# Optimization experiments

Measured on AMD Instinct MI355X. Metric: run time of the kernel, lower is better.

## Reference

```python
import jax, jax.numpy as jnp
import numpy as np
from jax import lax

RATE, STRIDE, KSIZE, FUSE_K, SCALE = 2, 1, 3, 3, 10.0


def img2col(img, k, s):
    # torch F.unfold with padding=1, reshaped to [B, L, C, k, k] (L row-major over patch grid)
    B, C, H, W = img.shape
    p = jnp.pad(img, ((0, 0), (0, 0), (1, 1), (1, 1)))
    nH = (H + 2 - k) // s + 1
    nW = (W + 2 - k) // s + 1
    slabs = [p[:, :, ki:ki + s * (nH - 1) + 1:s, kj:kj + s * (nW - 1) + 1:s]
             for ki in range(k) for kj in range(k)]
    pats = jnp.stack(slabs, axis=2).reshape(B, C, k, k, nH, nW)
    return pats.transpose(0, 4, 5, 1, 2, 3).reshape(B, nH * nW, C, k, k)


def diag_prop(M, fk):
    # conv2d of the [L, L] score matrix with an identity fuse kernel == sum over diagonal shifts
    r = fk // 2
    B, L, _ = M.shape
    Mp = jnp.pad(M, ((0, 0), (r, r), (r, r)))
    out = jnp.zeros_like(M)
    for d in range(-r, r + 1):
        out = out + Mp[:, r + d:r + d + L, r + d:r + d + L]
    return out


def _fwd(foreground, background, mask):
    pad = KSIZE // 2
    # raw-resolution background patches used for reconstruction: [B, L, C, 2*rate, 2*rate]
    cols = img2col(background, 2 * RATE, RATE * STRIDE)
    # nearest-neighbor downsample by rate (torch F.interpolate scale_factor=1/rate, mode='nearest')
    fg = foreground[:, :, ::RATE, ::RATE]
    bg = background[:, :, ::RATE, ::RATE]
    m = mask[:, :, ::RATE, ::RATE]
    mask_cols = img2col(m, KSIZE, STRIDE)            # [B, L, 1, 3, 3]
    masked = jnp.sum(mask_cols, axis=(2, 3, 4)) == 0.0  # [B, L]
    kern = img2col(bg, KSIZE, STRIDE)                # [B, L, C, 3, 3]
    denom = jnp.sqrt(jnp.sum(kern * kern, axis=(2, 3, 4), keepdims=True))
    kern = kern / jnp.maximum(denom, 1e-3)

    def conv_one(img, k_):  # img [C,h,w], k_ [L,C,3,3] -> [L,h,w]
        return lax.conv_general_dilated(img[None], k_, (1, 1), [(pad, pad), (pad, pad)],
                                        dimension_numbers=('NCHW', 'OIHW', 'NCHW'))[0]

    scores = jax.vmap(conv_one)(fg, kern)            # [B, L, h, w]
    B, L, h, w = scores.shape
    # attention propagation: identity-kernel conv over [h*w, h*w], both orientations
    M = diag_prop(scores.reshape(B, L, h * w), FUSE_K)
    M = M.reshape(B, h, w, h, w).transpose(0, 2, 1, 4, 3).reshape(B, h * w, h * w)
    M = diag_prop(M, FUSE_K)
    scores = M.reshape(B, h, w, h, w).transpose(0, 2, 1, 4, 3).reshape(B, L, h, w)
    scores = jnp.where(masked[:, :, None, None], -1000.0, scores)
    soft = jax.nn.softmax(SCALE * scores, axis=1)

    kt = 2 * RATE
    tpad = kt - 1 - pad  # conv_transpose2d(stride=rate, padding=pad) as dilated conv

    def deconv_one(s_, t_):  # s_ [L,h,w], t_ [L,C,kt,kt] -> [C,H,W]
        W2 = jnp.flip(jnp.transpose(t_, (1, 0, 2, 3)), (2, 3))  # [C,L,kt,kt]
        return lax.conv_general_dilated(s_[None], W2, (1, 1), [(tpad, tpad), (tpad, tpad)],
                                        lhs_dilation=(RATE, RATE),
                                        dimension_numbers=('NCHW', 'OIHW', 'NCHW'))[0]

    return jax.vmap(deconv_one)(soft, cols)          # [B, C, H, W]


def setup_inputs() -> dict:
    key = jax.random.key(0)
    kf, kb, km = jax.random.split(key, 3)
    B, C, H, W = 2, 64, 128, 128
    foreground = jax.random.normal(kf, (B, C, H, W), jnp.float32)
    background = jax.random.normal(kb, (B, C, H, W), jnp.float32)
    mask = (jax.random.uniform(km, (B, 1, H, W)) > 0.5).astype(jnp.float32)
    return {"foreground": foreground, "background": background, "mask": mask}


def reference(foreground, background, mask):
    return _fwd(foreground, background, mask)
```

## Files before the change

### kernel.cpp

```cpp
#include <hip/hip_runtime.h>
#include <hip/hip_bf16.h>

#define B_ 2
#define C_ 64
#define H_ 128
#define W_ 128
#define HS 64
#define WS 64
#define L_ 4096
#define S_ 4096
#define K1_ 576
#define NCOL 1024
#define SCALE_ 10.0f

typedef __attribute__((ext_vector_type(8))) short bf16x8;
typedef __attribute__((ext_vector_type(8))) _Float16 f16x8;
typedef __attribute__((ext_vector_type(4))) float f32x4;

__device__ __forceinline__ void async_copy16(const void* gsrc, void* ldst) {
    __builtin_amdgcn_global_load_lds(
        (__attribute__((address_space(1))) const void*)gsrc,
        (__attribute__((address_space(3))) void*)ldst, 16, 0, 0);
}

__device__ __forceinline__ int TT(int x) { return ((x & 63) << 6) | (x >> 6); }

__device__ __forceinline__ float diag3Y(const float* __restrict__ Y, int l, int s) {
    int tl = TT(l), ts = TT(s);
    float acc = 0.f;
#pragma unroll
    for (int d2 = -1; d2 <= 1; ++d2) {
        int p = tl + d2, q = ts + d2;
        if ((unsigned)p < 4096u && (unsigned)q < 4096u)
            acc += Y[((size_t)TT(p) << 12) + TT(q)];
    }
    return acc;
}

__global__ void k_sumsq(const float* __restrict__ bg, float* __restrict__ ssq) {
    int idx = blockIdx.x * 256 + threadIdx.x;
    if (idx >= B_ * HS * WS) return;
    int pix = idx & 4095, b = idx >> 12;
    int i = pix >> 6, j = pix & 63;
    float ss = 0.f;
    for (int c = 0; c < C_; ++c) {
        float v = bg[((b * C_ + c) * H_ + 2 * i) * W_ + 2 * j];
        ss += v * v;
    }
    ssq[idx] = ss;
}

__global__ void k_patch_stats(const float* __restrict__ mask, const float* __restrict__ ssq,
                              float* __restrict__ denom_inv, float* __restrict__ maskedf) {
    int idx = blockIdx.x * 256 + threadIdx.x;
    if (idx >= B_ * L_) return;
    int b = idx >> 12, l = idx & 4095, lh = l >> 6, lw = l & 63;
    float msum = 0.f, ss = 0.f;
    for (int di = -1; di <= 1; ++di)
        for (int dj = -1; dj <= 1; ++dj) {
            int i = lh + di, j = lw + dj;
            if (i >= 0 && i < HS && j >= 0 && j < WS) {
                msum += mask[(b * H_ + 2 * i) * W_ + 2 * j];
                ss += ssq[(b << 12) + (i << 6) + j];
            }
        }
    maskedf[idx] = (msum == 0.0f) ? 1.0f : 0.0f;
    denom_inv[idx] = 1.0f / fmaxf(sqrtf(ss), 0.001f);
}

__global__ void k_prep(const float* __restrict__ bgb, const float* __restrict__ fgb,
                       _Float16* __restrict__ bcol, _Float16* __restrict__ fcol,
                       __hip_bfloat16* __restrict__ colsT) {
    int idx = blockIdx.x * 256 + threadIdx.x;
    if (idx < 2 * L_ * K1_) {
        int which = idx >= L_ * K1_;
        int id = which ? idx - L_ * K1_ : idx;
        const float* src = which ? fgb : bgb;
        _Float16* dst = which ? fcol : bcol;
        int k = id % K1_;
        int l = id / K1_;
        int c = k / 9, r = k - 9 * c;
        int r3 = r / 3;
        int di = r3 - 1, dj = r - 3 * r3 - 1;
        int i = (l >> 6) + di, j = (l & 63) + dj;
        float v = 0.f;
        if (i >= 0 && i < HS && j >= 0 && j < WS) v = src[(c * H_ + 2 * i) * W_ + 2 * j];
        dst[id] = (_Float16)v;
    } else {
        int id = idx - 2 * L_ * K1_;
        int l = id & 4095, n = id >> 12;
        int kj = n & 3, ki = (n >> 2) & 3, c = n >> 4;
        int y = 2 * (l >> 6) + ki - 1, x = 2 * (l & 63) + kj - 1;
        float v = 0.f;
        if (y >= 0 && y < H_ && x >= 0 && x < W_) v = bgb[(c * H_ + y) * W_ + x];
        colsT[id] = __float2bfloat16(v);
    }
}

__global__ __launch_bounds__(256) void k_gemm1_mfma(const _Float16* __restrict__ A,
                                                    const _Float16* __restrict__ Bm,
                                                    const float* __restrict__ dinv,
                                                    float* __restrict__ scores,
                                                    float* __restrict__ Y) {
    __shared__ __align__(16) char shraw[65 * 129 * 4];
    _Float16* As = (_Float16*)shraw;
    _Float16* Bs = As + 8192;
    int t = threadIdx.x, lane = t & 63, w = t >> 6;
    int wm = w & 1, wn = w >> 1;
    int M0 = blockIdx.y * 128, N0 = blockIdx.x * 128;
    f32x4 acc[4][4] = {};
    for (int k0 = 0; k0 < K1_; k0 += 64) {
#pragma unroll
        for (int rp = 0; rp < 4; ++rp) {
            int chunk = rp * 256 + t;
            int row = chunk >> 3;
            int kc = (chunk & 7) ^ (row & 7);
            async_copy16(A + (size_t)(M0 + row) * K1_ + k0 + kc * 8, &As[chunk * 8]);
        }
#pragma unroll
        for (int rp = 0; rp < 4; ++rp) {
            int chunk = rp * 256 + t;
            int row = chunk >> 3;
            int kc = (chunk & 7) ^ (row & 7);
            async_copy16(Bm + (size_t)(N0 + row) * K1_ + k0 + kc * 8, &Bs[chunk * 8]);
        }
        __syncthreads();
        int qc = lane >> 4, mr = lane & 15;
#pragma unroll
        for (int kk = 0; kk < 2; ++kk) {
            int c = kk * 4 + qc;
            f16x8 af[4], bfr[4];
#pragma unroll
            for (int i = 0; i < 4; ++i) {
                int ra = wm * 64 + i * 16 + mr;
                int rb = wn * 64 + i * 16 + mr;
                af[i] = *(const f16x8*)&As[ra * 64 + (c ^ (ra & 7)) * 8];
                bfr[i] = *(const f16x8*)&Bs[rb * 64 + (c ^ (rb & 7)) * 8];
            }
#pragma unroll
            for (int mt = 0; mt < 4; ++mt)
#pragma unroll
                for (int nt = 0; nt < 4; ++nt)
                    acc[mt][nt] = __builtin_amdgcn_mfma_f32_16x16x32_f16(af[mt], bfr[nt], acc[mt][nt], 0, 0, 0);
        }
        __syncthreads();
    }
    int col = lane & 15, rq = (lane >> 4) * 4;
#pragma unroll
    for (int mt = 0; mt < 4; ++mt)
#pragma unroll
        for (int r = 0; r < 4; ++r) {
            int ml = wm * 64 + mt * 16 + rq + r;
            bool rstrip = (ml <= 1) || (ml >= 126);
            float dv = dinv[M0 + ml];
#pragma unroll
            for (int nt = 0; nt < 4; ++nt) {
                int nl = wn * 64 + nt * 16 + col;
                bool cstrip = (nl <= 1) || (nl >= 126);
                if (rstrip || cstrip)
                    scores[((size_t)(M0 + ml) << 12) + N0 + nl] = acc[mt][nt][r] * dv;
            }
        }
    float* sm = (float*)shraw;
#pragma unroll
    for (int pass = 0; pass < 2; ++pass) {
        int lo = pass * 63;
        __syncthreads();
#pragma unroll
        for (int mt = 0; mt < 4; ++mt)
#pragma unroll
            for (int r = 0; r < 4; ++r) {
                int ml = wm * 64 + mt * 16 + rq + r;
                if (ml >= lo && ml <= lo + 64) {
                    float dv = dinv[M0 + ml];
#pragma unroll
                    for (int nt = 0; nt < 4; ++nt) {
                        int nl = wn * 64 + nt * 16 + col;
                        sm[(ml - lo) * 129 + nl] = acc[mt][nt][r] * dv;
                    }
                }
            }
        __syncthreads();
        int r0 = pass == 0 ? 1 : 64;
        for (int e = t; e < 63 * 128; e += 256) {
            int rr = r0 + (e >> 7);
            int cc = e & 127;
            if (cc < 1 || cc > 126) continue;
            int li = rr - lo;
            float y = sm[(li - 1) * 129 + cc - 1] + sm[li * 129 + cc] + sm[(li + 1) * 129 + cc + 1];
            Y[((size_t)(M0 + rr) << 12) + N0 + cc] = y;
        }
    }
}

__global__ void k_pass1_edge(const float* __restrict__ scores, float* __restrict__ Y) {
    int idx = blockIdx.x * 256 + threadIdx.x;
    int a, c;
    if (idx < 262144) {
        int ri = idx >> 12;
        a = (ri >> 1) * 128 + ((ri & 1) ? 127 : 0);
        c = idx & 4095;
    } else {
        int j = idx - 262144;
        int ci = j >> 12;
        c = (ci >> 1) * 128 + ((ci & 1) ? 127 : 0);
        a = j & 4095;
    }
    float acc = 0.f;
#pragma unroll
    for (int d = -1; d <= 1; ++d) {
        int aa = a + d, cc = c + d;
        if ((unsigned)aa < 4096u && (unsigned)cc < 4096u)
            acc += scores[((size_t)aa << 12) + cc];
    }
    Y[((size_t)a << 12) + c] = acc;
}

__global__ __launch_bounds__(256) void k_soft3(const float* __restrict__ Y,
                                               const float* __restrict__ maskedf,
                                               __hip_bfloat16* __restrict__ softT,
                                               float* __restrict__ pml, float* __restrict__ pz) {
    __shared__ float tile[64][65];
    __shared__ float red[16][64];
    __shared__ float mloc[64];
    int t = threadIdx.x;
    int sx4 = t & 15, lg = t >> 4;
    int bid = blockIdx.x;
    int swz = (bid & 7) * 512 + (bid >> 3);
    int dg = swz >> 6, pos = swz & 63;
    int by = pos, bx = (pos + dg) & 63;
    int s0 = bx * 64, l0 = by * 64;
    bool interior = (bx >= 1) && (bx <= 62) && (by >= 1) && (by <= 62);
    float p0 = -3.0e38f, p1 = -3.0e38f, p2 = -3.0e38f, p3 = -3.0e38f;
    if (interior) {
        float4 v[12];
        float mk[4];
#pragma unroll
        for (int j = 0; j < 4; ++j) {
            int lloc = lg + 16 * j;
#pragma unroll
            for (int d2 = 0; d2 < 3; ++d2) {
                const float* p = Y + ((size_t)(64 * (by + d2 - 1) + lloc) << 12) + 64 * (bx + d2 - 1) + 4 * sx4;
                v[j * 3 + d2] = *(const float4*)p;
            }
        }
#pragma unroll
        for (int j = 0; j < 4; ++j) mk[j] = maskedf[l0 + lg + 16 * j];
#pragma unroll
        for (int j = 0; j < 4; ++j) {
            int lloc = lg + 16 * j;
            float a0 = v[j * 3].x + v[j * 3 + 1].x + v[j * 3 + 2].x;
            float a1 = v[j * 3].y + v[j * 3 + 1].y + v[j * 3 + 2].y;
            float a2 = v[j * 3].z + v[j * 3 + 1].z + v[j * 3 + 2].z;
            float a3 = v[j * 3].w + v[j * 3 + 1].w + v[j * 3 + 2].w;
            if (mk[j] != 0.f) { a0 = -1000.f; a1 = -1000.f; a2 = -1000.f; a3 = -1000.f; }
            tile[lloc][4 * sx4 + 0] = a0;
            tile[lloc][4 * sx4 + 1] = a1;
            tile[lloc][4 * sx4 + 2] = a2;
            tile[lloc][4 * sx4 + 3] = a3;
            p0 = fmaxf(p0, a0); p1 = fmaxf(p1, a1); p2 = fmaxf(p2, a2); p3 = fmaxf(p3, a3);
        }
    } else {
#pragma unroll
        for (int j = 0; j < 4; ++j) {
            int lloc = lg + 16 * j;
            int l = l0 + lloc;
            bool mk = (maskedf[l] != 0.f);
            float a0 = mk ? -1000.f : diag3Y(Y, l, s0 + 4 * sx4 + 0);
            float a1 = mk ? -1000.f : diag3Y(Y, l, s0 + 4 * sx4 + 1);
            float a2 = mk ? -1000.f : diag3Y(Y, l, s0 + 4 * sx4 + 2);
            float a3 = mk ? -1000.f : diag3Y(Y, l, s0 + 4 * sx4 + 3);
            tile[lloc][4 * sx4 + 0] = a0;
            tile[lloc][4 * sx4 + 1] = a1;
            tile[lloc][4 * sx4 + 2] = a2;
            tile[lloc][4 * sx4 + 3] = a3;
            p0 = fmaxf(p0, a0); p1 = fmaxf(p1, a1); p2 = fmaxf(p2, a2); p3 = fmaxf(p3, a3);
        }
    }
    red[lg][4 * sx4 + 0] = p0;
    red[lg][4 * sx4 + 1] = p1;
    red[lg][4 * sx4 + 2] = p2;
    red[lg][4 * sx4 + 3] = p3;
    __syncthreads();
    if (t < 64) {
        float m = -3.0e38f;
#pragma unroll
        for (int g = 0; g < 16; ++g) m = fmaxf(m, red[g][t]);
        mloc[t] = m;
        pml[(size_t)(s0 + t) * 64 + by] = m;
    }
    __syncthreads();
    float m0 = mloc[4 * sx4 + 0], m1 = mloc[4 * sx4 + 1], m2 = mloc[4 * sx4 + 2], m3 = mloc[4 * sx4 + 3];
    float z0 = 0.f, z1 = 0.f, z2 = 0.f, z3 = 0.f;
#pragma unroll
    for (int j = 0; j < 4; ++j) {
        int lloc = lg + 16 * j;
        float e0 = __expf(SCALE_ * (tile[lloc][4 * sx4 + 0] - m0));
        float e1 = __expf(SCALE_ * (tile[lloc][4 * sx4 + 1] - m1));
        float e2 = __expf(SCALE_ * (tile[lloc][4 * sx4 + 2] - m2));
        float e3 = __expf(SCALE_ * (tile[lloc][4 * sx4 + 3] - m3));
        tile[lloc][4 * sx4 + 0] = e0;
        tile[lloc][4 * sx4 + 1] = e1;
        tile[lloc][4 * sx4 + 2] = e2;
        tile[lloc][4 * sx4 + 3] = e3;
        z0 += e0; z1 += e1; z2 += e2; z3 += e3;
    }
    red[lg][4 * sx4 + 0] = z0;
    red[lg][4 * sx4 + 1] = z1;
    red[lg][4 * sx4 + 2] = z2;
    red[lg][4 * sx4 + 3] = z3;
    __syncthreads();
    if (t < 64) {
        float zz = 0.f;
#pragma unroll
        for (int g = 0; g < 16; ++g) zz += red[g][t];
        pz[(size_t)(s0 + t) * 64 + by] = zz;
    }
#pragma unroll
    for (int pp = 0; pp < 2; ++pp) {
        int chunk = pp * 256 + t;
        int sloc = chunk >> 3, lb = (chunk & 7) * 8;
        bf16x8 o;
#pragma unroll
        for (int k = 0; k < 8; ++k) {
            __hip_bfloat16 r = __float2bfloat16(tile[lb + k][sloc]);
            o[k] = *reinterpret_cast<short*>(&r);
        }
        *(bf16x8*)(softT + ((size_t)(s0 + sloc) << 12) + l0 + lb) = o;
    }
}

__global__ __launch_bounds__(256) void k_zr(const float* __restrict__ pml,
                                            const float* __restrict__ pz,
                                            __hip_bfloat16* __restrict__ softT) {
    __shared__ float facs[64];
    int t = threadIdx.x;
    int s = blockIdx.x;
    if (t < 64) {
        float pmv = pml[(size_t)s * 64 + t];
        float m = pmv;
#pragma unroll
        for (int off = 1; off < 64; off <<= 1) m = fmaxf(m, __shfl_xor(m, off));
        float fc = __expf(SCALE_ * (pmv - m));
        float g = pz[(size_t)s * 64 + t] * fc;
#pragma unroll
        for (int off = 1; off < 64; off <<= 1) g += __shfl_xor(g, off);
        facs[t] = fc * (1.0f / g);
    }
    __syncthreads();
    size_t rowbase = (size_t)s << 12;
#pragma unroll
    for (int p = 0; p < 2; ++p) {
        int chunk = t + p * 256;
        float f = facs[chunk >> 3];
        bf16x8 v = *(const bf16x8*)(softT + rowbase + chunk * 8);
        bf16x8 o;
#pragma unroll
        for (int k = 0; k < 8; ++k) {
            unsigned short us = (unsigned short)v[k];
            float x = __uint_as_float((unsigned)us << 16) * f;
            __hip_bfloat16 r = __float2bfloat16(x);
            o[k] = *reinterpret_cast<short*>(&r);
        }
        *(bf16x8*)(softT + rowbase + chunk * 8) = o;
    }
}

__global__ __launch_bounds__(256) void k_gemm2_mfma(const __hip_bfloat16* __restrict__ softT,
                                                    const __hip_bfloat16* __restrict__ colsT,
                                                    float* __restrict__ patchP) {
    __shared__ __hip_bfloat16 As[128 * 64], Bs[64 * 64];
    int t = threadIdx.x, lane = t & 63, w = t >> 6;
    int wm = w & 1, wn = w >> 1;
    int flat = blockIdx.x + (blockIdx.y << 4) + (blockIdx.z << 9);
    int xp = (flat >> 3) & 15;
    int yp = (flat & 7) | (((flat >> 7) & 3) << 3);
    int zp = flat >> 9;
    int M0 = yp * 128, N0 = xp * 64;
    int kbase = zp * 2048;
    f32x4 acc[4][2] = {};
    for (int k0 = kbase; k0 < kbase + 2048; k0 += 64) {
#pragma unroll
        for (int rp = 0; rp < 4; ++rp) {
            int chunk = rp * 256 + t;
            int row = chunk >> 3;
            int kc = (chunk & 7) ^ (row & 7);
            async_copy16(softT + ((size_t)(M0 + row) << 12) + k0 + kc * 8, &As[chunk * 8]);
        }
#pragma unroll
        for (int rp = 0; rp < 2; ++rp) {
            int chunk = rp * 256 + t;
            int row = chunk >> 3;
            int kc = (chunk & 7) ^ (row & 7);
            async_copy16(colsT + ((size_t)(N0 + row) << 12) + k0 + kc * 8, &Bs[chunk * 8]);
        }
        __syncthreads();
        int qc = lane >> 4, mr = lane & 15;
#pragma unroll
        for (int kk = 0; kk < 2; ++kk) {
            int c = kk * 4 + qc;
            bf16x8 af[4], bfr[2];
#pragma unroll
            for (int i = 0; i < 4; ++i) {
                int rowa = wm * 64 + i * 16 + mr;
                af[i] = *(const bf16x8*)&As[rowa * 64 + (c ^ (rowa & 7)) * 8];
            }
#pragma unroll
            for (int j = 0; j < 2; ++j) {
                int rowb = wn * 32 + j * 16 + mr;
                bfr[j] = *(const bf16x8*)&Bs[rowb * 64 + (c ^ (rowb & 7)) * 8];
            }
#pragma unroll
            for (int mt = 0; mt < 4; ++mt)
#pragma unroll
                for (int nt = 0; nt < 2; ++nt)
                    acc[mt][nt] = __builtin_amdgcn_mfma_f32_16x16x32_bf16(af[mt], bfr[nt], acc[mt][nt], 0, 0, 0);
        }
        __syncthreads();
    }
    float* P = patchP + ((size_t)zp << 22);
    int col = lane & 15, rq = (lane >> 4) * 4;
#pragma unroll
    for (int mt = 0; mt < 4; ++mt)
#pragma unroll
        for (int r = 0; r < 4; ++r) {
            int m = M0 + wm * 64 + mt * 16 + rq + r;
#pragma unroll
            for (int nt = 0; nt < 2; ++nt) {
                int n = N0 + wn * 32 + nt * 16 + col;
                P[(size_t)m * 1024 + n] = acc[mt][nt][r];
            }
        }
}

__global__ void k_col2im(const float* __restrict__ patchP, float* __restrict__ outb) {
    int idx = blockIdx.x * 256 + threadIdx.x;
    if (idx >= C_ * H_ * W_) return;
    int x = idx & 127, y = (idx >> 7) & 127, c = idx >> 14;
    const float* P0 = patchP;
    const float* P1 = patchP + (1u << 22);
    float acc = 0.f;
    int ki0 = (y + 1) & 1, kj0 = (x + 1) & 1;
#pragma unroll
    for (int ki = ki0; ki < 4; ki += 2) {
        int i = (y + 1 - ki) >> 1;
        if (i < 0 || i >= HS) continue;
#pragma unroll
        for (int kj = kj0; kj < 4; kj += 2) {
            int j = (x + 1 - kj) >> 1;
            if (j < 0 || j >= WS) continue;
            size_t off = ((size_t)(i * 64 + j) << 10) + c * 16 + ki * 4 + kj;
            acc += P0[off] + P1[off];
        }
    }
    outb[idx] = acc;
}

extern "C" void kernel_launch(void* const* d_in, const int* in_sizes, int n_in,
                              void* d_out, int out_size, void* d_ws, size_t ws_size,
                              hipStream_t stream) {
    (void)in_sizes; (void)n_in; (void)out_size; (void)ws_size;
    const float* fg = (const float*)d_in[0];
    const float* bg = (const float*)d_in[1];
    const float* mask = (const float*)d_in[2];
    float* out = (float*)d_out;

    float* ws = (float*)d_ws;
    float* scores = ws;
    float* patchP = ws;
    float* Y = ws + 16777216;
    _Float16* bgcol = (_Float16*)(ws + 33554432);
    _Float16* fgcol = (_Float16*)(ws + 34734080);
    __hip_bfloat16* softT = (__hip_bfloat16*)(ws + 38273024);
    __hip_bfloat16* colsT = (__hip_bfloat16*)(ws + 46661632);
    float* pml = ws + 48758784;
    float* pz = ws + 49020928;
    float* denom_inv = ws + 49283072;
    float* maskedf = ws + 49291264;
    float* ssq = ws + 49299456;

    k_sumsq<<<(B_ * HS * WS) / 256, 256, 0, stream>>>(bg, ssq);
    k_patch_stats<<<(B_ * L_) / 256, 256, 0, stream>>>(mask, ssq, denom_inv, maskedf);

    for (int b = 0; b < B_; ++b) {
        const float* bgb = bg + (size_t)b * C_ * H_ * W_;
        const float* fgb = fg + (size_t)b * C_ * H_ * W_;

        k_prep<<<(2 * L_ * K1_ + NCOL * L_) / 256, 256, 0, stream>>>(bgb, fgb, bgcol, fgcol, colsT);

        dim3 g1(32, 32);
        k_gemm1_mfma<<<g1, 256, 0, stream>>>(bgcol, fgcol, denom_inv + b * L_, scores, Y);
        k_pass1_edge<<<2048, 256, 0, stream>>>(scores, Y);

        k_soft3<<<4096, 256, 0, stream>>>(Y, maskedf + b * L_, softT, pml, pz);
        k_zr<<<4096, 256, 0, stream>>>(pml, pz, softT);

        dim3 g5(16, 32, 2);
        k_gemm2_mfma<<<g5, 256, 0, stream>>>(softT, colsT, patchP);
        k_col2im<<<(C_ * H_ * W_) / 256, 256, 0, stream>>>(patchP, out + (size_t)b * C_ * H_ * W_);
    }
}
```

Baseline: 443.9 us.

## Double-buffer LDS tiles in both MFMA GEMMs with async prefetch

Both GEMM kernels now prefetch the next K tile into a second LDS buffer via global_load_lds while computing on the current one, using manual vmcnt waits and raw s_barrier instead of __syncthreads. In gemm1 the enlarged LDS buffer also lets the diagonal-sum epilogue run in a single pass over the whole 128x128 tile instead of two half passes. This aims to hide global load latency behind MFMA work. The cost is larger LDS use per block (about 66KB for gemm1, 48KB for gemm2), which may reduce occupancy, and correctness now depends on the hand-written vmcnt counts.

```diff
diff --git a/kernel.cpp b/kernel.cpp
--- a/kernel.cpp
+++ b/kernel.cpp
@@ -102,29 +102,43 @@
                                                     const float* __restrict__ dinv,
                                                     float* __restrict__ scores,
                                                     float* __restrict__ Y) {
-    __shared__ __align__(16) char shraw[65 * 129 * 4];
-    _Float16* As = (_Float16*)shraw;
-    _Float16* Bs = As + 8192;
+    __shared__ __align__(16) char shraw[128 * 129 * 4];
     int t = threadIdx.x, lane = t & 63, w = t >> 6;
     int wm = w & 1, wn = w >> 1;
     int M0 = blockIdx.y * 128, N0 = blockIdx.x * 128;
     f32x4 acc[4][4] = {};
-    for (int k0 = 0; k0 < K1_; k0 += 64) {
+
+    auto stage = [&](int k0, int offh) {
+        _Float16* Asb = (_Float16*)shraw + offh;
+        _Float16* Bsb = Asb + 8192;
 #pragma unroll
         for (int rp = 0; rp < 4; ++rp) {
             int chunk = rp * 256 + t;
             int row = chunk >> 3;
             int kc = (chunk & 7) ^ (row & 7);
-            async_copy16(A + (size_t)(M0 + row) * K1_ + k0 + kc * 8, &As[chunk * 8]);
+            async_copy16(A + (size_t)(M0 + row) * K1_ + k0 + kc * 8, &Asb[chunk * 8]);
         }
 #pragma unroll
         for (int rp = 0; rp < 4; ++rp) {
             int chunk = rp * 256 + t;
             int row = chunk >> 3;
             int kc = (chunk & 7) ^ (row & 7);
-            async_copy16(Bm + (size_t)(N0 + row) * K1_ + k0 + kc * 8, &Bs[chunk * 8]);
-        }
-        __syncthreads();
+            async_copy16(Bm + (size_t)(N0 + row) * K1_ + k0 + kc * 8, &Bsb[chunk * 8]);
+        }
+    };
+
+    stage(0, 0);
+    int buf = 0;
+    for (int k0 = 0; k0 < K1_; k0 += 64) {
+        if (k0 + 64 < K1_) {
+            stage(k0 + 64, (buf ^ 1) * 16384);
+            asm volatile("s_waitcnt vmcnt(8)" ::: "memory");
+        } else {
+            asm volatile("s_waitcnt vmcnt(0)" ::: "memory");
+        }
+        __builtin_amdgcn_s_barrier();
+        _Float16* As = (_Float16*)shraw + buf * 16384;
+        _Float16* Bs = As + 8192;
         int qc = lane >> 4, mr = lane & 15;
 #pragma unroll
         for (int kk = 0; kk < 2; ++kk) {
@@ -143,7 +157,8 @@
                 for (int nt = 0; nt < 4; ++nt)
                     acc[mt][nt] = __builtin_amdgcn_mfma_f32_16x16x32_f16(af[mt], bfr[nt], acc[mt][nt], 0, 0, 0);
         }
-        __syncthreads();
+        __builtin_amdgcn_s_barrier();
+        buf ^= 1;
     }
     int col = lane & 15, rq = (lane >> 4) * 4;
 #pragma unroll
@@ -163,33 +178,24 @@
         }
     float* sm = (float*)shraw;
 #pragma unroll
-    for (int pass = 0; pass < 2; ++pass) {
-        int lo = pass * 63;
-        __syncthreads();
-#pragma unroll
-        for (int mt = 0; mt < 4; ++mt)
-#pragma unroll
-            for (int r = 0; r < 4; ++r) {
-                int ml = wm * 64 + mt * 16 + rq + r;
-                if (ml >= lo && ml <= lo + 64) {
-                    float dv = dinv[M0 + ml];
-#pragma unroll
-                    for (int nt = 0; nt < 4; ++nt) {
-                        int nl = wn * 64 + nt * 16 + col;
-                        sm[(ml - lo) * 129 + nl] = acc[mt][nt][r] * dv;
-                    }
-                }
-            }
-        __syncthreads();
-        int r0 = pass == 0 ? 1 : 64;
-        for (int e = t; e < 63 * 128; e += 256) {
-            int rr = r0 + (e >> 7);
-            int cc = e & 127;
-            if (cc < 1 || cc > 126) continue;
-            int li = rr - lo;
-            float y = sm[(li - 1) * 129 + cc - 1] + sm[li * 129 + cc] + sm[(li + 1) * 129 + cc + 1];
-            Y[((size_t)(M0 + rr) << 12) + N0 + cc] = y;
-        }
+    for (int mt = 0; mt < 4; ++mt)
+#pragma unroll
+        for (int r = 0; r < 4; ++r) {
+            int ml = wm * 64 + mt * 16 + rq + r;
+            float dv = dinv[M0 + ml];
+#pragma unroll
+            for (int nt = 0; nt < 4; ++nt) {
+                int nl = wn * 64 + nt * 16 + col;
+                sm[ml * 129 + nl] = acc[mt][nt][r] * dv;
+            }
+        }
+    __syncthreads();
+    for (int e = t; e < 126 * 128; e += 256) {
+        int rr = 1 + (e >> 7);
+        int cc = e & 127;
+        if (cc < 1 || cc > 126) continue;
+        float y = sm[(rr - 1) * 129 + cc - 1] + sm[rr * 129 + cc] + sm[(rr + 1) * 129 + cc + 1];
+        Y[((size_t)(M0 + rr) << 12) + N0 + cc] = y;
     }
 }
 
@@ -369,7 +375,7 @@
 __global__ __launch_bounds__(256) void k_gemm2_mfma(const __hip_bfloat16* __restrict__ softT,
                                                     const __hip_bfloat16* __restrict__ colsT,
                                                     float* __restrict__ patchP) {
-    __shared__ __hip_bfloat16 As[128 * 64], Bs[64 * 64];
+    __shared__ __hip_bfloat16 AsB[2][12288];
     int t = threadIdx.x, lane = t & 63, w = t >> 6;
     int wm = w & 1, wn = w >> 1;
     int flat = blockIdx.x + (blockIdx.y << 4) + (blockIdx.z << 9);
@@ -379,22 +385,38 @@
     int M0 = yp * 128, N0 = xp * 64;
     int kbase = zp * 2048;
     f32x4 acc[4][2] = {};
-    for (int k0 = kbase; k0 < kbase + 2048; k0 += 64) {
+
+    auto stage = [&](int k0, int bsel) {
+        __hip_bfloat16* Asb = AsB[bsel];
+        __hip_bfloat16* Bsb = Asb + 8192;
 #pragma unroll
         for (int rp = 0; rp < 4; ++rp) {
             int chunk = rp * 256 + t;
             int row = chunk >> 3;
             int kc = (chunk & 7) ^ (row & 7);
-            async_copy16(softT + ((size_t)(M0 + row) << 12) + k0 + kc * 8, &As[chunk * 8]);
+            async_copy16(softT + ((size_t)(M0 + row) << 12) + k0 + kc * 8, &Asb[chunk * 8]);
         }
 #pragma unroll
         for (int rp = 0; rp < 2; ++rp) {
             int chunk = rp * 256 + t;
             int row = chunk >> 3;
             int kc = (chunk & 7) ^ (row & 7);
-            async_copy16(colsT + ((size_t)(N0 + row) << 12) + k0 + kc * 8, &Bs[chunk * 8]);
-        }
-        __syncthreads();
+            async_copy16(colsT + ((size_t)(N0 + row) << 12) + k0 + kc * 8, &Bsb[chunk * 8]);
+        }
+    };
+
+    stage(kbase, 0);
+    int buf = 0;
+    for (int k0 = kbase; k0 < kbase + 2048; k0 += 64) {
+        if (k0 + 64 < kbase + 2048) {
+            stage(k0 + 64, buf ^ 1);
+            asm volatile("s_waitcnt vmcnt(6)" ::: "memory");
+        } else {
+            asm volatile("s_waitcnt vmcnt(0)" ::: "memory");
+        }
+        __builtin_amdgcn_s_barrier();
+        __hip_bfloat16* As = AsB[buf];
+        __hip_bfloat16* Bs = As + 8192;
         int qc = lane >> 4, mr = lane & 15;
 #pragma unroll
         for (int kk = 0; kk < 2; ++kk) {
@@ -416,7 +438,8 @@
                 for (int nt = 0; nt < 2; ++nt)
                     acc[mt][nt] = __builtin_amdgcn_mfma_f32_16x16x32_bf16(af[mt], bfr[nt], acc[mt][nt], 0, 0, 0);
         }
-        __syncthreads();
+        __builtin_amdgcn_s_barrier();
+        buf ^= 1;
     }
     float* P = patchP + ((size_t)zp << 22);
     int col = lane & 15, rq = (lane >> 4) * 4;
```

Measured after the change: 443.0 us. Within noise of the previous version (-0.2%).

## Double-buffer GEMM1 LDS tiles with async prefetch and BK=32

Applied to the files above, without the earlier changes.

Restructures the score GEMM main loop to double-buffer the A and B tiles in LDS. The K step drops to 32 and the next tile is prefetched with async global-to-LDS loads while MFMAs run on the current one, synchronised with vmcnt waits and barriers. The LDS swizzle is changed to match the narrower 32-wide rows, and s_setprio is raised around the MFMA block. This is meant to hide global load latency that the single-buffered loop exposed, at the cost of more loop iterations and barriers.

```diff
diff --git a/kernel.cpp b/kernel.cpp
--- a/kernel.cpp
+++ b/kernel.cpp
@@ -103,47 +103,60 @@
                                                     float* __restrict__ scores,
                                                     float* __restrict__ Y) {
     __shared__ __align__(16) char shraw[65 * 129 * 4];
-    _Float16* As = (_Float16*)shraw;
-    _Float16* Bs = As + 8192;
     int t = threadIdx.x, lane = t & 63, w = t >> 6;
     int wm = w & 1, wn = w >> 1;
     int M0 = blockIdx.y * 128, N0 = blockIdx.x * 128;
     f32x4 acc[4][4] = {};
-    for (int k0 = 0; k0 < K1_; k0 += 64) {
-#pragma unroll
-        for (int rp = 0; rp < 4; ++rp) {
+
+    auto stage = [&](int k0, int bsel) {
+        _Float16* Asb = (_Float16*)shraw + bsel * 8192;
+        _Float16* Bsb = Asb + 4096;
+#pragma unroll
+        for (int rp = 0; rp < 2; ++rp) {
             int chunk = rp * 256 + t;
-            int row = chunk >> 3;
-            int kc = (chunk & 7) ^ (row & 7);
-            async_copy16(A + (size_t)(M0 + row) * K1_ + k0 + kc * 8, &As[chunk * 8]);
-        }
-#pragma unroll
-        for (int rp = 0; rp < 4; ++rp) {
+            int row = chunk >> 2;
+            int kc = (chunk & 3) ^ ((row >> 1) & 3);
+            async_copy16(A + (size_t)(M0 + row) * K1_ + k0 + kc * 8, &Asb[chunk * 8]);
+        }
+#pragma unroll
+        for (int rp = 0; rp < 2; ++rp) {
             int chunk = rp * 256 + t;
-            int row = chunk >> 3;
-            int kc = (chunk & 7) ^ (row & 7);
-            async_copy16(Bm + (size_t)(N0 + row) * K1_ + k0 + kc * 8, &Bs[chunk * 8]);
-        }
-        __syncthreads();
-        int qc = lane >> 4, mr = lane & 15;
-#pragma unroll
-        for (int kk = 0; kk < 2; ++kk) {
-            int c = kk * 4 + qc;
-            f16x8 af[4], bfr[4];
-#pragma unroll
-            for (int i = 0; i < 4; ++i) {
-                int ra = wm * 64 + i * 16 + mr;
-                int rb = wn * 64 + i * 16 + mr;
-                af[i] = *(const f16x8*)&As[ra * 64 + (c ^ (ra & 7)) * 8];
-                bfr[i] = *(const f16x8*)&Bs[rb * 64 + (c ^ (rb & 7)) * 8];
-            }
-#pragma unroll
-            for (int mt = 0; mt < 4; ++mt)
-#pragma unroll
-                for (int nt = 0; nt < 4; ++nt)
-                    acc[mt][nt] = __builtin_amdgcn_mfma_f32_16x16x32_f16(af[mt], bfr[nt], acc[mt][nt], 0, 0, 0);
-        }
-        __syncthreads();
+            int row = chunk >> 2;
+            int kc = (chunk & 3) ^ ((row >> 1) & 3);
+            async_copy16(Bm + (size_t)(N0 + row) * K1_ + k0 + kc * 8, &Bsb[chunk * 8]);
+        }
+    };
+
+    stage(0, 0);
+    int buf = 0;
+    int qc = lane >> 4, mr = lane & 15;
+    for (int k0 = 0; k0 < K1_; k0 += 32) {
+        if (k0 + 32 < K1_) {
+            stage(k0 + 32, buf ^ 1);
+            asm volatile("s_waitcnt vmcnt(4)" ::: "memory");
+        } else {
+            asm volatile("s_waitcnt vmcnt(0)" ::: "memory");
+        }
+        __builtin_amdgcn_s_barrier();
+        _Float16* As = (_Float16*)shraw + buf * 8192;
+        _Float16* Bs = As + 4096;
+        f16x8 af[4], bfr[4];
+#pragma unroll
+        for (int i = 0; i < 4; ++i) {
+            int ra = wm * 64 + i * 16 + mr;
+            int rb = wn * 64 + i * 16 + mr;
+            af[i] = *(const f16x8*)&As[ra * 32 + (qc ^ ((ra >> 1) & 3)) * 8];
+            bfr[i] = *(const f16x8*)&Bs[rb * 32 + (qc ^ ((rb >> 1) & 3)) * 8];
+        }
+        __builtin_amdgcn_s_setprio(1);
+#pragma unroll
+        for (int mt = 0; mt < 4; ++mt)
+#pragma unroll
+            for (int nt = 0; nt < 4; ++nt)
+                acc[mt][nt] = __builtin_amdgcn_mfma_f32_16x16x32_f16(af[mt], bfr[nt], acc[mt][nt], 0, 0, 0);
+        __builtin_amdgcn_s_setprio(0);
+        __builtin_amdgcn_s_barrier();
+        buf ^= 1;
     }
     int col = lane & 15, rq = (lane >> 4) * 4;
 #pragma unroll
```

Measured after the change: 444.7 us. About the same (+0.2%).
